# Kernel optimization log

Hardware: AMD Instinct MI355X
Metric: run time of the kernel (lower is better)

## Reference

```python
import jax, jax.numpy as jnp
import numpy as np

N = 50000       # nodes
E = 600000      # edges (avg degree 12)
F_IN = 64       # input_bands
F_HID = 128     # 2 * input_bands
F_OUT = 128     # output_bands
EPS = 1e-5      # BatchNorm eps


def setup_inputs() -> dict:
    key = jax.random.key(0)
    ks = jax.random.split(key, 12)
    x = jax.random.normal(ks[0], (N, F_IN), jnp.float32)
    edge_index = jax.random.randint(ks[1], (2, E), 0, N, dtype=jnp.int32)
    # GCNConv weight (glorot-ish) and bias
    W1 = jax.random.normal(ks[2], (F_IN, F_HID), jnp.float32) / np.sqrt(F_IN)
    b1 = jnp.zeros((F_HID,), jnp.float32)
    gamma1 = jnp.ones((F_HID,), jnp.float32)
    beta1 = jnp.zeros((F_HID,), jnp.float32)
    # SAGEConv: lin_l (aggregated neighbors, with bias), lin_r (root, no bias)
    Wl = jax.random.normal(ks[3], (F_HID, F_OUT), jnp.float32) / np.sqrt(F_HID)
    bl = jnp.zeros((F_OUT,), jnp.float32)
    Wr = jax.random.normal(ks[4], (F_HID, F_OUT), jnp.float32) / np.sqrt(F_HID)
    gamma2 = jnp.ones((F_OUT,), jnp.float32)
    beta2 = jnp.zeros((F_OUT,), jnp.float32)
    return {"x": x, "edge_index": edge_index, "W1": W1, "b1": b1,
            "gamma1": gamma1, "beta1": beta1, "Wl": Wl, "bl": bl,
            "Wr": Wr, "gamma2": gamma2, "beta2": beta2}


def _bn_train(h, gamma, beta):
    # BatchNorm1d in training mode: biased batch stats over the node axis
    mean = h.mean(axis=0)
    var = h.var(axis=0)
    return gamma * (h - mean) * jax.lax.rsqrt(var + EPS) + beta


def _gcn_conv(x, src, dst, W, b):
    # PyG GCNConv: x' = D^{-1/2}(A + I)D^{-1/2} X W + b
    h = x @ W                                   # [N, F_HID]
    loop = jnp.arange(N, dtype=src.dtype)
    src_sl = jnp.concatenate([src, loop])       # self-loops appended
    dst_sl = jnp.concatenate([dst, loop])
    deg = jax.ops.segment_sum(jnp.ones(E + N, h.dtype), dst_sl, num_segments=N)
    dis = jnp.where(deg > 0, jax.lax.rsqrt(deg), 0.0)  # deg^{-1/2}, inf -> 0
    norm = dis[src_sl] * dis[dst_sl]            # [E+N]
    msg = h[src_sl] * norm[:, None]             # gather + scale
    return jax.ops.segment_sum(msg, dst_sl, num_segments=N) + b


def _sage_conv(x, src, dst, Wl, bl, Wr):
    # PyG SAGEConv (mean aggr): x' = lin_l(mean_{j in N(i)} x_j) + lin_r(x_i)
    cnt = jax.ops.segment_sum(jnp.ones(E, x.dtype), dst, num_segments=N)
    neigh = jax.ops.segment_sum(x[src], dst, num_segments=N)
    neigh = neigh / jnp.maximum(cnt, 1.0)[:, None]
    return neigh @ Wl + bl + x @ Wr


def reference(x, edge_index, W1, b1, gamma1, beta1, Wl, bl, Wr, gamma2, beta2):
    src, dst = edge_index[0], edge_index[1]
    h = _gcn_conv(x, src, dst, W1, b1)
    h = jax.nn.relu(_bn_train(h, gamma1, beta1))  # dropout = identity (eval)
    h = _sage_conv(h, src, dst, Wl, bl, Wr)
    h = jax.nn.relu(_bn_train(h, gamma2, beta2))
    return h
```

## Files before the change

kernel.cpp:

```cpp
#include <hip/hip_runtime.h>

#define NN 50000
#define NE 600000
#define FIN 64
#define FHID 128
#define BN_EPS 1e-5f
#define CAP 64

typedef __attribute__((ext_vector_type(8))) short short8;
typedef __attribute__((ext_vector_type(4))) float f32x4;

__device__ __forceinline__ unsigned short f2bf(float f) {
  unsigned u = __float_as_uint(f);
  return (unsigned short)((u + 0x7FFFu + ((u >> 16) & 1u)) >> 16);
}
__device__ __forceinline__ float bfs(unsigned short u) {
  return __uint_as_float(((unsigned)u) << 16);
}
__device__ __forceinline__ float bflo(unsigned v) { return __uint_as_float(v << 16); }
__device__ __forceinline__ float bfhi(unsigned v) { return __uint_as_float(v & 0xFFFF0000u); }
__device__ __forceinline__ unsigned pk2(float lo, float hi) {
  return (unsigned)f2bf(lo) | ((unsigned)f2bf(hi) << 16);
}

__global__ __launch_bounds__(256) void bucket_fill(const int* __restrict__ src,
                                                   const int* __restrict__ dst,
                                                   int* __restrict__ cnt,
                                                   int* __restrict__ csr) {
  int e = blockIdx.x * 256 + threadIdx.x;
  if (e < NE) {
    int d = dst[e];
    int p = atomicAdd(&cnt[d], 1);
    if (p < CAP) csr[(size_t)d * CAP + p] = src[e];
  }
}

__global__ __launch_bounds__(256) void scale_x(const float* __restrict__ x,
                                               const int* __restrict__ cnt,
                                               ushort4* __restrict__ xs) {
  int i = blockIdx.x * 256 + threadIdx.x;
  float4 v = ((const float4*)x)[i];
  int node = i >> 4;
  float d = rsqrtf((float)(cnt[node] + 1));
  xs[i] = make_ushort4(f2bf(v.x * d), f2bf(v.y * d), f2bf(v.z * d), f2bf(v.w * d));
}

__device__ __forceinline__ void gacc(float& a0, float& a1, float& a2, float& a3,
                                     ushort4 v) {
  a0 += bfs(v.x); a1 += bfs(v.y); a2 += bfs(v.z); a3 += bfs(v.w);
}

__global__ __launch_bounds__(256) void gcn_agg(const unsigned short* __restrict__ xs,
                                               const int* __restrict__ csr,
                                               const int* __restrict__ cnt,
                                               unsigned short* __restrict__ xa) {
  int tid = threadIdx.x;
  int node = blockIdx.x * 16 + (tid >> 4);
  int li = tid & 15;
  int deg = cnt[node];
  int degc = min(deg, CAP);
  float di = rsqrtf((float)(deg + 1));
  ushort4 sv = *(const ushort4*)(xs + (size_t)node * FIN + li * 4);
  float a0 = bfs(sv.x), a1 = bfs(sv.y), a2 = bfs(sv.z), a3 = bfs(sv.w);
  const int* cb = csr + (size_t)node * CAP;
  int e = 0;
  for (; e + 8 <= degc; e += 8) {
    int4 sA = *(const int4*)(cb + e);
    int4 sB = *(const int4*)(cb + e + 4);
    ushort4 v0 = *(const ushort4*)(xs + (size_t)sA.x * FIN + li * 4);
    ushort4 v1 = *(const ushort4*)(xs + (size_t)sA.y * FIN + li * 4);
    ushort4 v2 = *(const ushort4*)(xs + (size_t)sA.z * FIN + li * 4);
    ushort4 v3 = *(const ushort4*)(xs + (size_t)sA.w * FIN + li * 4);
    ushort4 v4 = *(const ushort4*)(xs + (size_t)sB.x * FIN + li * 4);
    ushort4 v5 = *(const ushort4*)(xs + (size_t)sB.y * FIN + li * 4);
    ushort4 v6 = *(const ushort4*)(xs + (size_t)sB.z * FIN + li * 4);
    ushort4 v7 = *(const ushort4*)(xs + (size_t)sB.w * FIN + li * 4);
    gacc(a0, a1, a2, a3, v0); gacc(a0, a1, a2, a3, v1);
    gacc(a0, a1, a2, a3, v2); gacc(a0, a1, a2, a3, v3);
    gacc(a0, a1, a2, a3, v4); gacc(a0, a1, a2, a3, v5);
    gacc(a0, a1, a2, a3, v6); gacc(a0, a1, a2, a3, v7);
  }
  for (; e + 4 <= degc; e += 4) {
    int4 sA = *(const int4*)(cb + e);
    ushort4 v0 = *(const ushort4*)(xs + (size_t)sA.x * FIN + li * 4);
    ushort4 v1 = *(const ushort4*)(xs + (size_t)sA.y * FIN + li * 4);
    ushort4 v2 = *(const ushort4*)(xs + (size_t)sA.z * FIN + li * 4);
    ushort4 v3 = *(const ushort4*)(xs + (size_t)sA.w * FIN + li * 4);
    gacc(a0, a1, a2, a3, v0); gacc(a0, a1, a2, a3, v1);
    gacc(a0, a1, a2, a3, v2); gacc(a0, a1, a2, a3, v3);
  }
  for (; e < degc; ++e) {
    ushort4 v = *(const ushort4*)(xs + (size_t)cb[e] * FIN + li * 4);
    gacc(a0, a1, a2, a3, v);
  }
  ushort4 o = make_ushort4(f2bf(di * a0), f2bf(di * a1), f2bf(di * a2), f2bf(di * a3));
  *(ushort4*)(xa + (size_t)node * FIN + li * 4) = o;
}

__device__ __forceinline__ void sacc(float* a, uint4 v) {
  a[0] += bflo(v.x); a[1] += bfhi(v.x);
  a[2] += bflo(v.y); a[3] += bfhi(v.y);
  a[4] += bflo(v.z); a[5] += bfhi(v.z);
  a[6] += bflo(v.w); a[7] += bfhi(v.w);
}

__global__ __launch_bounds__(256) void sage_agg(const unsigned* __restrict__ hb,
                                                const int* __restrict__ csr,
                                                const int* __restrict__ cnt,
                                                unsigned* __restrict__ neighb) {
  int tid = threadIdx.x;
  int node = blockIdx.x * 16 + (tid >> 4);
  int li = tid & 15;
  int deg = cnt[node];
  int degc = min(deg, CAP);
  float a[8];
#pragma unroll
  for (int i = 0; i < 8; ++i) a[i] = 0.f;
  const int* cb = csr + (size_t)node * CAP;
  int e = 0;
  for (; e + 8 <= degc; e += 8) {
    int4 sA = *(const int4*)(cb + e);
    int4 sB = *(const int4*)(cb + e + 4);
    uint4 v0 = *(const uint4*)(hb + (size_t)sA.x * 64 + li * 4);
    uint4 v1 = *(const uint4*)(hb + (size_t)sA.y * 64 + li * 4);
    uint4 v2 = *(const uint4*)(hb + (size_t)sA.z * 64 + li * 4);
    uint4 v3 = *(const uint4*)(hb + (size_t)sA.w * 64 + li * 4);
    uint4 v4 = *(const uint4*)(hb + (size_t)sB.x * 64 + li * 4);
    uint4 v5 = *(const uint4*)(hb + (size_t)sB.y * 64 + li * 4);
    uint4 v6 = *(const uint4*)(hb + (size_t)sB.z * 64 + li * 4);
    uint4 v7 = *(const uint4*)(hb + (size_t)sB.w * 64 + li * 4);
    sacc(a, v0); sacc(a, v1); sacc(a, v2); sacc(a, v3);
    sacc(a, v4); sacc(a, v5); sacc(a, v6); sacc(a, v7);
  }
  for (; e + 4 <= degc; e += 4) {
    int4 sA = *(const int4*)(cb + e);
    uint4 v0 = *(const uint4*)(hb + (size_t)sA.x * 64 + li * 4);
    uint4 v1 = *(const uint4*)(hb + (size_t)sA.y * 64 + li * 4);
    uint4 v2 = *(const uint4*)(hb + (size_t)sA.z * 64 + li * 4);
    uint4 v3 = *(const uint4*)(hb + (size_t)sA.w * 64 + li * 4);
    sacc(a, v0); sacc(a, v1); sacc(a, v2); sacc(a, v3);
  }
  for (; e < degc; ++e) {
    uint4 v = *(const uint4*)(hb + (size_t)cb[e] * 64 + li * 4);
    sacc(a, v);
  }
  float inv = 1.0f / fmaxf((float)deg, 1.0f);
  uint4 o;
  o.x = pk2(a[0] * inv, a[1] * inv);
  o.y = pk2(a[2] * inv, a[3] * inv);
  o.z = pk2(a[4] * inv, a[5] * inv);
  o.w = pk2(a[6] * inv, a[7] * inv);
  *(uint4*)(neighb + (size_t)node * 64 + li * 4) = o;
}

template <int K1, int K2, bool OUTBF>
__global__ __launch_bounds__(256) void gemm_mfma(const short* __restrict__ A1,
                                                 const short* __restrict__ A2,
                                                 const float* __restrict__ B1,
                                                 const float* __restrict__ B2,
                                                 const float* __restrict__ bias,
                                                 float* __restrict__ Cf,
                                                 unsigned short* __restrict__ Cb,
                                                 float* __restrict__ sums,
                                                 float* __restrict__ sumsq) {
  constexpr int KT = K1 + K2;
  __shared__ short Bt[128][KT + 8];
  __shared__ float lsum[128], lsq[128];
  int tid = threadIdx.x;
  if (tid < 128) { lsum[tid] = 0.f; lsq[tid] = 0.f; }
  for (int idx = tid; idx < KT * 128; idx += 256) {
    int k = idx >> 7, n = idx & 127;
    float wv = (K2 == 0 || k < K1) ? B1[k * 128 + n] : B2[(k - K1) * 128 + n];
    Bt[n][k] = (short)f2bf(wv);
  }
  __syncthreads();

  int lane = tid & 63;
  int w = tid >> 6;
  int r = lane & 15;
  int q = lane >> 4;
  int row_base = blockIdx.x * 128 + w * 32;

  f32x4 acc[2][8];
#pragma unroll
  for (int m = 0; m < 2; ++m)
#pragma unroll
    for (int n = 0; n < 8; ++n) acc[m][n] = (f32x4){0.f, 0.f, 0.f, 0.f};

#pragma unroll
  for (int seg = 0; seg < 2; ++seg) {
    const int K = seg ? K2 : K1;
    if (K == 0) continue;
    const short* A = seg ? A2 : A1;
    const int kb = seg ? K1 : 0;
    for (int ks = 0; ks < K; ks += 32) {
      int row0 = row_base + r;
      int row1 = row_base + 16 + r;
      row0 = row0 < NN ? row0 : NN - 1;
      row1 = row1 < NN ? row1 : NN - 1;
      short8 af0 = *(const short8*)(A + (size_t)row0 * K + ks + q * 8);
      short8 af1 = *(const short8*)(A + (size_t)row1 * K + ks + q * 8);
#pragma unroll
      for (int n = 0; n < 8; ++n) {
        short8 bf = *(const short8*)(&Bt[n * 16 + r][kb + ks + q * 8]);
        acc[0][n] = __builtin_amdgcn_mfma_f32_16x16x32_bf16(af0, bf, acc[0][n], 0, 0, 0);
        acc[1][n] = __builtin_amdgcn_mfma_f32_16x16x32_bf16(af1, bf, acc[1][n], 0, 0, 0);
      }
    }
  }

  float bias_r[8];
#pragma unroll
  for (int n = 0; n < 8; ++n) bias_r[n] = bias[n * 16 + r];
  float cs[8], cq[8];
#pragma unroll
  for (int n = 0; n < 8; ++n) { cs[n] = 0.f; cq[n] = 0.f; }
#pragma unroll
  for (int m = 0; m < 2; ++m)
#pragma unroll
    for (int i = 0; i < 4; ++i) {
      int row = row_base + m * 16 + q * 4 + i;
      if (row < NN) {
#pragma unroll
        for (int n = 0; n < 8; ++n) {
          float v = acc[m][n][i] + bias_r[n];
          int col = n * 16 + r;
          if constexpr (OUTBF)
            Cb[(size_t)row * 128 + col] = f2bf(v);
          else
            Cf[(size_t)row * 128 + col] = v;
          cs[n] += v;
          cq[n] += v * v;
        }
      }
    }
#pragma unroll
  for (int n = 0; n < 8; ++n) {
    atomicAdd(&lsum[n * 16 + r], cs[n]);
    atomicAdd(&lsq[n * 16 + r], cq[n]);
  }
  __syncthreads();
  if (tid < 128) {
    atomicAdd(&sums[tid], lsum[tid]);
    atomicAdd(&sumsq[tid], lsq[tid]);
  }
}

__global__ __launch_bounds__(256) void bn_apply_bf(unsigned* __restrict__ hb,
                                                   const float* __restrict__ sums,
                                                   const float* __restrict__ sumsq,
                                                   const float* __restrict__ gamma,
                                                   const float* __restrict__ beta) {
  __shared__ float sc[128], sh[128];
  int t = threadIdx.x;
  if (t < 128) {
    float mean = sums[t] * (1.0f / NN);
    float var = fmaxf(sumsq[t] * (1.0f / NN) - mean * mean, 0.f);
    float inv = rsqrtf(var + BN_EPS);
    float s = gamma[t] * inv;
    sc[t] = s;
    sh[t] = beta[t] - mean * s;
  }
  __syncthreads();
  int i = blockIdx.x * 256 + t;
  uint2 v = ((uint2*)hb)[i];
  int c = (i & 31) * 4;
  float f0 = fmaxf(fmaf(bflo(v.x), sc[c + 0], sh[c + 0]), 0.f);
  float f1 = fmaxf(fmaf(bfhi(v.x), sc[c + 1], sh[c + 1]), 0.f);
  float f2 = fmaxf(fmaf(bflo(v.y), sc[c + 2], sh[c + 2]), 0.f);
  float f3 = fmaxf(fmaf(bfhi(v.y), sc[c + 3], sh[c + 3]), 0.f);
  v.x = (unsigned)f2bf(f0) | ((unsigned)f2bf(f1) << 16);
  v.y = (unsigned)f2bf(f2) | ((unsigned)f2bf(f3) << 16);
  ((uint2*)hb)[i] = v;
}

__global__ __launch_bounds__(256) void bn_apply_f32(float* __restrict__ out,
                                                    const float* __restrict__ sums,
                                                    const float* __restrict__ sumsq,
                                                    const float* __restrict__ gamma,
                                                    const float* __restrict__ beta) {
  __shared__ float sc[128], sh[128];
  int t = threadIdx.x;
  if (t < 128) {
    float mean = sums[t] * (1.0f / NN);
    float var = fmaxf(sumsq[t] * (1.0f / NN) - mean * mean, 0.f);
    float inv = rsqrtf(var + BN_EPS);
    float s = gamma[t] * inv;
    sc[t] = s;
    sh[t] = beta[t] - mean * s;
  }
  __syncthreads();
  int i4 = blockIdx.x * 256 + t;
  float4 v = ((const float4*)out)[i4];
  int f = (i4 & 31) * 4;
  v.x = fmaxf(fmaf(v.x, sc[f + 0], sh[f + 0]), 0.f);
  v.y = fmaxf(fmaf(v.y, sc[f + 1], sh[f + 1]), 0.f);
  v.z = fmaxf(fmaf(v.z, sc[f + 2], sh[f + 2]), 0.f);
  v.w = fmaxf(fmaf(v.w, sc[f + 3], sh[f + 3]), 0.f);
  ((float4*)out)[i4] = v;
}

extern "C" void kernel_launch(void* const* d_in, const int* in_sizes, int n_in,
                              void* d_out, int out_size, void* d_ws, size_t ws_size,
                              hipStream_t stream) {
  const float* x   = (const float*)d_in[0];
  const int*   ei  = (const int*)d_in[1];
  const float* W1  = (const float*)d_in[2];
  const float* b1  = (const float*)d_in[3];
  const float* g1  = (const float*)d_in[4];
  const float* be1 = (const float*)d_in[5];
  const float* Wl  = (const float*)d_in[6];
  const float* bl  = (const float*)d_in[7];
  const float* Wr  = (const float*)d_in[8];
  const float* g2  = (const float*)d_in[9];
  const float* be2 = (const float*)d_in[10];
  const int* srcp = ei;
  const int* dstp = ei + NE;

  char* w = (char*)d_ws;
  auto alloc = [&](size_t bytes) {
    char* p = w;
    w += (bytes + 255) & ~(size_t)255;
    return p;
  };
  int*   cnt     = (int*)alloc((size_t)NN * 4);
  int*   csr     = (int*)alloc((size_t)NN * CAP * 4);
  unsigned short* xs     = (unsigned short*)alloc((size_t)NN * FIN * 2);
  unsigned short* xa     = (unsigned short*)alloc((size_t)NN * FIN * 2);
  unsigned short* hb     = (unsigned short*)alloc((size_t)NN * FHID * 2);
  unsigned*       neighb = (unsigned*)alloc((size_t)NN * FHID * 2);
  float* stats   = (float*)alloc(8 * 128 * 4);
  float* sums1 = stats,       *sumsq1 = stats + 128;
  float* sums2 = stats + 512, *sumsq2 = stats + 640;

  hipMemsetAsync(cnt, 0, (size_t)NN * 4, stream);
  hipMemsetAsync(stats, 0, 8 * 128 * 4, stream);

  int nbE = (NE + 255) / 256;
  int nbA = NN / 16;
  int nbG = (NN + 127) / 128;

  bucket_fill<<<nbE, 256, 0, stream>>>(srcp, dstp, cnt, csr);
  scale_x<<<NN * FIN / 4 / 256, 256, 0, stream>>>(x, cnt, (ushort4*)xs);

  gcn_agg<<<nbA, 256, 0, stream>>>(xs, csr, cnt, xa);
  gemm_mfma<64, 0, true><<<nbG, 256, 0, stream>>>(
      (const short*)xa, nullptr, W1, nullptr, b1, nullptr, hb, sums1, sumsq1);
  bn_apply_bf<<<NN * FHID / 4 / 256, 256, 0, stream>>>((unsigned*)hb, sums1, sumsq1,
                                                       g1, be1);

  sage_agg<<<nbA, 256, 0, stream>>>((const unsigned*)hb, csr, cnt, neighb);
  gemm_mfma<128, 128, false><<<nbG, 256, 0, stream>>>(
      (const short*)neighb, (const short*)hb, Wl, Wr, bl, (float*)d_out, nullptr,
      sums2, sumsq2);
  bn_apply_f32<<<NN * FHID / 4 / 256, 256, 0, stream>>>((float*)d_out, sums2, sumsq2,
                                                        g2, be2);
}
```

Measured before the change: 235.5 us.

## Pack GEMM weights into MFMA fragment layout and preload all A fragments

Weights are staged into shared memory in a lane-contiguous layout that matches the MFMA B-fragment order, so each lane reads 16 contiguous bytes without bank conflicts, and the global weight loads become float4 reads. All A fragments for the full K extent are loaded into registers up front, so global loads are issued together ahead of the MFMA loop. This raises register pressure (up to 16 short8 values for K=256) and may lower occupancy.

```diff
diff --git a/kernel.cpp b/kernel.cpp
--- a/kernel.cpp
+++ b/kernel.cpp
@@ -164,14 +164,24 @@
                                                  float* __restrict__ sums,
                                                  float* __restrict__ sumsq) {
   constexpr int KT = K1 + K2;
-  __shared__ short Bt[128][KT + 8];
+  constexpr int NK1 = K1 / 32;
+  constexpr int NKS = KT / 32;
+  __shared__ short Bp[8 * NKS * 64 * 8];
   __shared__ float lsum[128], lsq[128];
   int tid = threadIdx.x;
   if (tid < 128) { lsum[tid] = 0.f; lsq[tid] = 0.f; }
-  for (int idx = tid; idx < KT * 128; idx += 256) {
-    int k = idx >> 7, n = idx & 127;
-    float wv = (K2 == 0 || k < K1) ? B1[k * 128 + n] : B2[(k - K1) * 128 + n];
-    Bt[n][k] = (short)f2bf(wv);
+  for (int idx = tid; idx < KT * 32; idx += 256) {
+    int k = idx >> 5, c4 = idx & 31;
+    const float* Bsrc = (K2 == 0 || k < K1) ? (B1 + k * 128) : (B2 + (k - K1) * 128);
+    float4 wv = *(const float4*)(Bsrc + c4 * 4);
+    int ks = k >> 5, q = (k >> 3) & 3, kk = k & 7;
+#pragma unroll
+    for (int j = 0; j < 4; ++j) {
+      int c = c4 * 4 + j;
+      int nf = c >> 4, r = c & 15;
+      float wj = j == 0 ? wv.x : (j == 1 ? wv.y : (j == 2 ? wv.z : wv.w));
+      Bp[((nf * NKS + ks) * 64 + q * 16 + r) * 8 + kk] = (short)f2bf(wj);
+    }
   }
   __syncthreads();
 
@@ -180,6 +190,20 @@
   int r = lane & 15;
   int q = lane >> 4;
   int row_base = blockIdx.x * 128 + w * 32;
+  int row0 = row_base + r;
+  int row1 = row_base + 16 + r;
+  row0 = row0 < NN ? row0 : NN - 1;
+  row1 = row1 < NN ? row1 : NN - 1;
+
+  short8 af[2][NKS];
+#pragma unroll
+  for (int ks = 0; ks < NKS; ++ks) {
+    const short* A = (K2 == 0 || ks < NK1) ? A1 : A2;
+    const int Kw = (K2 == 0 || ks < NK1) ? K1 : K2;
+    const int ko = ((K2 == 0 || ks < NK1) ? ks : ks - NK1) * 32;
+    af[0][ks] = *(const short8*)(A + (size_t)row0 * Kw + ko + q * 8);
+    af[1][ks] = *(const short8*)(A + (size_t)row1 * Kw + ko + q * 8);
+  }
 
   f32x4 acc[2][8];
 #pragma unroll
@@ -188,24 +212,12 @@
     for (int n = 0; n < 8; ++n) acc[m][n] = (f32x4){0.f, 0.f, 0.f, 0.f};
 
 #pragma unroll
-  for (int seg = 0; seg < 2; ++seg) {
-    const int K = seg ? K2 : K1;
-    if (K == 0) continue;
-    const short* A = seg ? A2 : A1;
-    const int kb = seg ? K1 : 0;
-    for (int ks = 0; ks < K; ks += 32) {
-      int row0 = row_base + r;
-      int row1 = row_base + 16 + r;
-      row0 = row0 < NN ? row0 : NN - 1;
-      row1 = row1 < NN ? row1 : NN - 1;
-      short8 af0 = *(const short8*)(A + (size_t)row0 * K + ks + q * 8);
-      short8 af1 = *(const short8*)(A + (size_t)row1 * K + ks + q * 8);
-#pragma unroll
-      for (int n = 0; n < 8; ++n) {
-        short8 bf = *(const short8*)(&Bt[n * 16 + r][kb + ks + q * 8]);
-        acc[0][n] = __builtin_amdgcn_mfma_f32_16x16x32_bf16(af0, bf, acc[0][n], 0, 0, 0);
-        acc[1][n] = __builtin_amdgcn_mfma_f32_16x16x32_bf16(af1, bf, acc[1][n], 0, 0, 0);
-      }
+  for (int ks = 0; ks < NKS; ++ks) {
+#pragma unroll
+    for (int n = 0; n < 8; ++n) {
+      short8 bf = *(const short8*)(Bp + ((size_t)(n * NKS + ks) * 64 + lane) * 8);
+      acc[0][n] = __builtin_amdgcn_mfma_f32_16x16x32_bf16(af[0][ks], bf, acc[0][n], 0, 0, 0);
+      acc[1][n] = __builtin_amdgcn_mfma_f32_16x16x32_bf16(af[1][ks], bf, acc[1][n], 0, 0, 0);
     }
   }
 
```

After: 238.5 us. Within noise of the previous version (+1.3%).
